# Kernel tuning notes

Measured on AMD Instinct MI355X. Metric: run time of the kernel, lower is better.

Reference implementation:

```python
import jax, jax.numpy as jnp
import numpy as np

BN_EPS = 1e-5

def conv1x1(x_bcn, w, b):
    # x: [B,C,N], w: [O,C], b: [O] -> [B,O,N]
    return jnp.einsum('oc,bcn->bon', w, x_bcn) + b[None, :, None]

def bn_eval(x, g, b):
    # inference BN with running_mean=0, running_var=1
    return x / jnp.sqrt(1.0 + BN_EPS) * g + b

def setup_inputs() -> dict:
    key = jax.random.key(0)
    ks = jax.random.split(key, 24)
    B, C, H, W = 2, 256, 64, 64
    Cq = C // 4
    s = lambda k, sh, fan: jax.random.normal(k, sh, jnp.float32) * (1.0 / np.sqrt(fan))
    inp = {
        'input1': jax.random.normal(ks[0], (B, C, H, W), jnp.float32),
        'input2': jax.random.normal(ks[1], (B, C, H, W), jnp.float32),
        'q1_w': s(ks[2], (Cq, C), C), 'q1_b': jnp.zeros((Cq,), jnp.float32),
        'k1_w': s(ks[3], (Cq, C), C), 'k1_b': jnp.zeros((Cq,), jnp.float32),
        'v1_w': s(ks[4], (C, C), C),  'v1_b': jnp.zeros((C,), jnp.float32),
        'q2_w': s(ks[5], (Cq, C), C), 'q2_b': jnp.zeros((Cq,), jnp.float32),
        'k2_w': s(ks[6], (Cq, C), C), 'k2_b': jnp.zeros((Cq,), jnp.float32),
        'v2_w': s(ks[7], (C, C), C),  'v2_b': jnp.zeros((C,), jnp.float32),
        'g1_w': s(ks[8], (C, 2 * C), 2 * C), 'g1_b': jnp.zeros((C,), jnp.float32),
        'bn1_g': jnp.ones((C,), jnp.float32), 'bn1_b': jnp.zeros((C,), jnp.float32),
        'g2_w': s(ks[9], (Cq, C), C), 'g2_b': jnp.zeros((Cq,), jnp.float32),
        'bn2_g': jnp.ones((Cq,), jnp.float32), 'bn2_b': jnp.zeros((Cq,), jnp.float32),
        'gamma': jnp.zeros((1,), jnp.float32) + 0.5,  # nonzero so attention branch matters
    }
    return inp

def _attshare(input1, input2, q1_w, q1_b, k1_w, k1_b, v1_w, v1_b,
              q2_w, q2_b, k2_w, k2_b, v2_w, v2_b,
              g1_w, g1_b, bn1_g, bn1_b, g2_w, g2_b, bn2_g, bn2_b, gamma):
    B, C, H, W = input1.shape
    N = H * W
    x1 = input1.reshape(B, C, N)
    x2 = input2.reshape(B, C, N)
    # global attention branch: adaptive avg pool -> conv -> BN -> relu -> conv -> BN -> sigmoid
    pooled = jnp.concatenate([x1, x2], axis=1).mean(axis=2)          # [B, 2C]
    y = jnp.einsum('oc,bc->bo', g1_w, pooled) + g1_b
    y = jax.nn.relu(bn_eval(y, bn1_g, bn1_b))
    y = jnp.einsum('oc,bc->bo', g2_w, y) + g2_b
    g = jax.nn.sigmoid(bn_eval(y, bn2_g, bn2_b))                      # [B, C/4]

    def stream(x, inp4d, qw, qb, kw, kb, vw, vb):
        q = conv1x1(x, qw, qb).transpose(0, 2, 1)   # [B, N, C/4]
        k = conv1x1(x, kw, kb)                       # [B, C/4, N]
        v = conv1x1(x, vw, vb)                       # [B, C, N]
        # bmm(q, g.repeat(N)) has identical columns -> per-row bias
        bias = jnp.einsum('bnc,bc->bn', q, g)        # [B, N]
        attn = jnp.einsum('bnc,bcm->bnm', q, k) + bias[:, :, None]
        attn = jax.nn.softmax(attn, axis=-1)         # [B, N, N]
        out = jnp.einsum('bcj,bij->bci', v, attn)    # [B, C, N]
        return gamma * out.reshape(inp4d.shape) + inp4d

    out1 = stream(x1, input1, q1_w, q1_b, k1_w, k1_b, v1_w, v1_b)
    out2 = stream(x2, input2, q2_w, q2_b, k2_w, k2_b, v2_w, v2_b)
    return out1, out2

def reference(input1, input2, q1_w, q1_b, k1_w, k1_b, v1_w, v1_b,
              q2_w, q2_b, k2_w, k2_b, v2_w, v2_b,
              g1_w, g1_b, bn1_g, bn1_b, g2_w, g2_b, bn2_g, bn2_b, gamma):
    return _attshare(input1, input2, q1_w, q1_b, k1_w, k1_b, v1_w, v1_b,
                     q2_w, q2_b, k2_w, k2_b, v2_w, v2_b,
                     g1_w, g1_b, bn1_g, bn1_b, g2_w, g2_b, bn2_g, bn2_b, gamma)
```

## Files before the change

### kernel.cpp

```cpp
#include <hip/hip_runtime.h>
#include <math.h>

constexpr int B_  = 2;
constexpr int C_  = 256;
constexpr int CQ_ = 64;
constexpr int N_  = 4096;

typedef __attribute__((ext_vector_type(8))) short     short8;
typedef __attribute__((ext_vector_type(8))) _Float16  half8;
typedef __attribute__((ext_vector_type(4))) float     f32x4;

constexpr float SHIFT = 24.0f;

static __device__ __forceinline__ unsigned short f2bf(float x) {
    union { float f; unsigned u; } v; v.f = x;
    unsigned r = (v.u + 0x7FFFu + ((v.u >> 16) & 1u)) >> 16;
    return (unsigned short)r;
}

__global__ __launch_bounds__(256)
void wconv_kernel(const float* __restrict__ q1w, const float* __restrict__ k1w,
                  const float* __restrict__ v1w, const float* __restrict__ q2w,
                  const float* __restrict__ k2w, const float* __restrict__ v2w,
                  _Float16* __restrict__ wb)
{
    int i = (blockIdx.x * 256 + threadIdx.x) * 4;
    const float* src;
    int off;
    if      (i < 16384)  { src = q1w; off = 0; }
    else if (i < 32768)  { src = k1w; off = 16384; }
    else if (i < 98304)  { src = v1w; off = 32768; }
    else if (i < 114688) { src = q2w; off = 98304; }
    else if (i < 131072) { src = k2w; off = 114688; }
    else                 { src = v2w; off = 131072; }
    float4 f = *(const float4*)(src + (i - off));
    _Float16 h0 = (_Float16)f.x, h1 = (_Float16)f.y;
    _Float16 h2 = (_Float16)f.z, h3 = (_Float16)f.w;
    ushort4 u;
    u.x = *(unsigned short*)&h0; u.y = *(unsigned short*)&h1;
    u.z = *(unsigned short*)&h2; u.w = *(unsigned short*)&h3;
    *(ushort4*)((unsigned short*)wb + i) = u;
}

__global__ __launch_bounds__(512)
void proj_kernel(const float* __restrict__ in1, const float* __restrict__ in2,
                 const _Float16* __restrict__ wb,
                 const float* __restrict__ q1b, const float* __restrict__ k1b,
                 const float* __restrict__ v1b, const float* __restrict__ q2b,
                 const float* __restrict__ k2b, const float* __restrict__ v2b,
                 _Float16* __restrict__ q_ws, _Float16* __restrict__ kf_ws,
                 unsigned short* __restrict__ vf_ws)
{
    __shared__ _Float16 Xs[64 * 264];
    const int bs = blockIdx.y, s = bs >> 1, bb = bs & 1;
    const int n0 = blockIdx.x * 64;
    const float* x = (s ? in2 : in1) + (size_t)bb * C_ * N_;
    const int tid = threadIdx.x;
    const int lane = tid & 63, wave = tid >> 6, quad = lane >> 4, l15 = lane & 15;

    #pragma unroll
    for (int rep = 0; rep < 8; ++rep) {
        int idx = rep * 512 + tid;
        int c = idx >> 4, ng = idx & 15;
        float4 f = *(const float4*)(x + (size_t)c * N_ + n0 + ng * 4);
        Xs[(ng * 4 + 0) * 264 + c] = (_Float16)f.x;
        Xs[(ng * 4 + 1) * 264 + c] = (_Float16)f.y;
        Xs[(ng * 4 + 2) * 264 + c] = (_Float16)f.z;
        Xs[(ng * 4 + 3) * 264 + c] = (_Float16)f.w;
    }
    __syncthreads();

    const _Float16* wqs = wb + (size_t)s * 98304;
    const _Float16* wks = wqs + 16384;
    const _Float16* wvs = wks + 16384;

    {
        const int m = wave >> 2, nb = wave & 3;
        const _Float16* W = m ? wks : wqs;
        const float* bias = m ? (s ? k2b : k1b) : (s ? q2b : q1b);
        half8 af[8];
        #pragma unroll
        for (int kh = 0; kh < 8; ++kh)
            af[kh] = *(const half8*)(&Xs[(16 * nb + l15) * 264 + quad * 8 + kh * 32]);
        f32x4 a4[4];
        #pragma unroll
        for (int o = 0; o < 4; ++o) a4[o] = (f32x4){0.f, 0.f, 0.f, 0.f};
        #pragma unroll
        for (int kh = 0; kh < 8; ++kh)
            #pragma unroll
            for (int o = 0; o < 4; ++o) {
                half8 bf = *(const half8*)(W + (size_t)(16 * o + l15) * C_ + quad * 8 + kh * 32);
                a4[o] = __builtin_amdgcn_mfma_f32_16x16x32_f16(af[kh], bf, a4[o], 0, 0, 0);
            }
        if (m == 0) {
            _Float16* outp = q_ws + (size_t)bs * N_ * CQ_;
            #pragma unroll
            for (int o = 0; o < 4; ++o) {
                float bv = bias[16 * o + l15];
                #pragma unroll
                for (int r = 0; r < 4; ++r) {
                    int n = n0 + 16 * nb + quad * 4 + r;
                    outp[(size_t)n * CQ_ + 16 * o + l15] = (_Float16)(a4[o][r] + bv);
                }
            }
        } else {
            unsigned short* kd = (unsigned short*)(kf_ws) + (size_t)bs * 262144;
            const int jt = (n0 >> 4) + nb;
            const int e = l15 & 7;
            #pragma unroll
            for (int o = 0; o < 4; ++o) {
                float bv = bias[16 * o + l15];
                const int kh = o >> 1;
                const int lhi = ((o & 1) * 2 + (l15 >> 3)) * 16;
                #pragma unroll
                for (int r = 0; r < 4; ++r) {
                    _Float16 hv = (_Float16)(a4[o][r] + bv);
                    int lane_f = lhi + quad * 4 + r;
                    kd[(size_t)(jt * 2 + kh) * 512 + lane_f * 8 + e] = *(unsigned short*)&hv;
                }
            }
        }
    }

    {
        const float* vb = s ? v2b : v1b;
        unsigned short* vd = vf_ws + (size_t)bs * 1048576;
        f32x4 v4[2][4];
        #pragma unroll
        for (int o = 0; o < 2; ++o)
            #pragma unroll
            for (int nt = 0; nt < 4; ++nt) v4[o][nt] = (f32x4){0.f, 0.f, 0.f, 0.f};
        #pragma unroll
        for (int kh = 0; kh < 8; ++kh) {
            half8 bf[4], af[2];
            #pragma unroll
            for (int nt = 0; nt < 4; ++nt)
                bf[nt] = *(const half8*)(&Xs[(16 * nt + l15) * 264 + quad * 8 + kh * 32]);
            #pragma unroll
            for (int o = 0; o < 2; ++o)
                af[o] = *(const half8*)(wvs + (size_t)(32 * wave + 16 * o + l15) * C_ + quad * 8 + kh * 32);
            #pragma unroll
            for (int o = 0; o < 2; ++o)
                #pragma unroll
                for (int nt = 0; nt < 4; ++nt)
                    v4[o][nt] = __builtin_amdgcn_mfma_f32_16x16x32_f16(af[o], bf[nt], v4[o][nt], 0, 0, 0);
        }
        const int e = l15 & 7;
        #pragma unroll
        for (int o = 0; o < 2; ++o) {
            const int ct = 2 * wave + o;
            #pragma unroll
            for (int r = 0; r < 4; ++r) {
                int c = 32 * wave + 16 * o + quad * 4 + r;
                float bv = vb[c];
                #pragma unroll
                for (int nt = 0; nt < 4; ++nt) {
                    const int j32 = (n0 >> 5) + (nt >> 1);
                    const int lane_f = ((nt & 1) * 2 + (l15 >> 3)) * 16 + quad * 4 + r;
                    vd[(size_t)(j32 * 16 + ct) * 512 + lane_f * 8 + e] =
                        f2bf(v4[o][nt][r] + bv);
                }
            }
        }
    }
}

__global__ __launch_bounds__(1024)
void flash_kernel(const _Float16* __restrict__ qg,
                  const _Float16* __restrict__ kfg,
                  const unsigned short* __restrict__ vfg,
                  const float* __restrict__ in1, const float* __restrict__ in2,
                  const float* __restrict__ gamma_p, float* __restrict__ out)
{
    __shared__ unsigned short Pt[2][64 * 64];
    __shared__ float lsum[64 * 4];

    const int tid  = threadIdx.x;
    const int lane = tid & 63;
    const int wave = tid >> 6;
    const int quad = lane >> 4;
    const int l15  = lane & 15;
    const int bs   = blockIdx.x & 3;
    const int q0   = (blockIdx.x >> 2) * 64;
    const int s = bs >> 1, bb = bs & 1;
    const int jsub  = wave & 3;
    const int ihalf = (wave >> 2) & 1;
    const int wc = wave & 7;
    const int jh = wave >> 3;

    const _Float16* qp = qg + (size_t)bs * N_ * CQ_;
    const _Float16* kB = kfg + (size_t)bs * 262144 + lane * 8;
    const unsigned short* vB = vfg + (size_t)bs * 1048576 + (size_t)lane * 8;

    unsigned char* ptb0 = (unsigned char*)&Pt[0][0];
    unsigned char* ptb1 = (unsigned char*)&Pt[1][0];

    half8 qf[2][2];
    float lacc[2] = {0.f, 0.f};
    half8 kf[2];
    short8 vf[2];
    f32x4 acc[4][2];
    #pragma unroll
    for (int a = 0; a < 4; ++a)
        #pragma unroll
        for (int bq = 0; bq < 2; ++bq) acc[a][bq] = (f32x4){0.f, 0.f, 0.f, 0.f};

    if (wave < 8) {
        #pragma unroll
        for (int isub = 0; isub < 2; ++isub)
            #pragma unroll
            for (int kh = 0; kh < 2; ++kh)
                qf[isub][kh] = *(const half8*)(
                    qp + (size_t)(q0 + 32 * ihalf + 16 * isub + l15) * CQ_ + quad * 8 + kh * 32);
        kf[0] = *(const half8*)(kB + (size_t)(jsub * 2 + 0) * 512);
        kf[1] = *(const half8*)(kB + (size_t)(jsub * 2 + 1) * 512);
        f32x4 sacc[2];
        sacc[0] = (f32x4){0.f, 0.f, 0.f, 0.f};
        sacc[1] = (f32x4){0.f, 0.f, 0.f, 0.f};
        #pragma unroll
        for (int kh = 0; kh < 2; ++kh)
            #pragma unroll
            for (int isub = 0; isub < 2; ++isub)
                sacc[isub] = __builtin_amdgcn_mfma_f32_16x16x32_f16(
                    kf[kh], qf[isub][kh], sacc[isub], 0, 0, 0);
        #pragma unroll
        for (int isub = 0; isub < 2; ++isub) {
            f32x4 p;
            p.x = __expf(sacc[isub].x - SHIFT);
            p.y = __expf(sacc[isub].y - SHIFT);
            p.z = __expf(sacc[isub].z - SHIFT);
            p.w = __expf(sacc[isub].w - SHIFT);
            lacc[isub] += p.x + p.y + p.z + p.w;
            unsigned pk0, pk1;
            asm("v_cvt_pk_bf16_f32 %0, %1, %2" : "=v"(pk0) : "v"(p.x), "v"(p.y));
            asm("v_cvt_pk_bf16_f32 %0, %1, %2" : "=v"(pk1) : "v"(p.z), "v"(p.w));
            int row = 32 * ihalf + 16 * isub + l15;
            int cb  = (32 * jsub + 8 * quad) ^ ((row & 7) << 4);
            uint2 pbv; pbv.x = pk0; pbv.y = pk1;
            *(uint2*)(ptb0 + row * 128 + cb) = pbv;
        }
        kf[0] = *(const half8*)(kB + (size_t)((4 + jsub) * 2 + 0) * 512);
        kf[1] = *(const half8*)(kB + (size_t)((4 + jsub) * 2 + 1) * 512);
    }
    vf[0] = *(const short8*)(vB + (size_t)(jh * 16 + 2 * wc + 0) * 512);
    vf[1] = *(const short8*)(vB + (size_t)(jh * 16 + 2 * wc + 1) * 512);

    for (int t = 0; t < 64; ++t) {
        unsigned char* ptr = (t & 1) ? ptb1 : ptb0;
        unsigned char* ptw = (t & 1) ? ptb0 : ptb1;

        asm volatile("s_waitcnt lgkmcnt(0)" ::: "memory");
        __builtin_amdgcn_sched_barrier(0);
        __builtin_amdgcn_s_barrier();
        __builtin_amdgcn_sched_barrier(0);

        short8 ap[4];
        #pragma unroll
        for (int is2 = 0; is2 < 4; ++is2) {
            int row = 16 * is2 + l15;
            int cb  = (jh * 64 + quad * 16) ^ ((row & 7) << 4);
            ap[is2] = *(const short8*)(ptr + row * 128 + cb);
        }
        __builtin_amdgcn_s_setprio(1);
        #pragma unroll
        for (int is2 = 0; is2 < 4; ++is2)
            #pragma unroll
            for (int csub = 0; csub < 2; ++csub)
                acc[is2][csub] = __builtin_amdgcn_mfma_f32_16x16x32_bf16(
                    ap[is2], vf[csub], acc[is2][csub], 0, 0, 0);
        __builtin_amdgcn_s_setprio(0);

        if (t < 63) {
            if (wave < 8) {
                f32x4 sacc[2];
                sacc[0] = (f32x4){0.f, 0.f, 0.f, 0.f};
                sacc[1] = (f32x4){0.f, 0.f, 0.f, 0.f};
                #pragma unroll
                for (int kh = 0; kh < 2; ++kh)
                    #pragma unroll
                    for (int isub = 0; isub < 2; ++isub)
                        sacc[isub] = __builtin_amdgcn_mfma_f32_16x16x32_f16(
                            kf[kh], qf[isub][kh], sacc[isub], 0, 0, 0);
                #pragma unroll
                for (int isub = 0; isub < 2; ++isub) {
                    f32x4 p;
                    p.x = __expf(sacc[isub].x - SHIFT);
                    p.y = __expf(sacc[isub].y - SHIFT);
                    p.z = __expf(sacc[isub].z - SHIFT);
                    p.w = __expf(sacc[isub].w - SHIFT);
                    lacc[isub] += p.x + p.y + p.z + p.w;
                    unsigned pk0, pk1;
                    asm("v_cvt_pk_bf16_f32 %0, %1, %2" : "=v"(pk0) : "v"(p.x), "v"(p.y));
                    asm("v_cvt_pk_bf16_f32 %0, %1, %2" : "=v"(pk1) : "v"(p.z), "v"(p.w));
                    int row = 32 * ihalf + 16 * isub + l15;
                    int cb  = (32 * jsub + 8 * quad) ^ ((row & 7) << 4);
                    uint2 pbv; pbv.x = pk0; pbv.y = pk1;
                    *(uint2*)(ptw + row * 128 + cb) = pbv;
                }
                int tk = (t + 2) & 63;
                kf[0] = *(const half8*)(kB + (size_t)((tk * 4 + jsub) * 2 + 0) * 512);
                kf[1] = *(const half8*)(kB + (size_t)((tk * 4 + jsub) * 2 + 1) * 512);
            }
            vf[0] = *(const short8*)(vB + (size_t)((2 * (t + 1) + jh) * 16 + 2 * wc + 0) * 512);
            vf[1] = *(const short8*)(vB + (size_t)((2 * (t + 1) + jh) * 16 + 2 * wc + 1) * 512);
        }
    }

    if (wave < 8) {
        #pragma unroll
        for (int isub = 0; isub < 2; ++isub) {
            float t = lacc[isub];
            t += __shfl_xor(t, 16);
            t += __shfl_xor(t, 32);
            if (quad == 0)
                lsum[(32 * ihalf + 16 * isub + l15) * 4 + jsub] = t;
        }
    }
    __syncthreads();

    float* red = (float*)&Pt[0][0];
    #pragma unroll
    for (int r = 0; r < 4; ++r) {
        if (wave >= 8) {
            *(f32x4*)(red + (size_t)(wave - 8) * 512 + lane * 8 + 0) = acc[r][0];
            *(f32x4*)(red + (size_t)(wave - 8) * 512 + lane * 8 + 4) = acc[r][1];
        }
        __syncthreads();
        if (wave < 8) {
            f32x4 a0 = *(const f32x4*)(red + (size_t)wave * 512 + lane * 8 + 0);
            f32x4 a1 = *(const f32x4*)(red + (size_t)wave * 512 + lane * 8 + 4);
            acc[r][0] += a0;
            acc[r][1] += a1;
        }
        __syncthreads();
    }

    if (wave < 8) {
        const float gamma = gamma_p[0];
        const float* inp = (s ? in2 : in1) + (size_t)bb * C_ * N_;
        float* op = out + (size_t)bs * C_ * N_;
        #pragma unroll
        for (int is2 = 0; is2 < 4; ++is2) {
            float inv[4];
            #pragma unroll
            for (int r = 0; r < 4; ++r) {
                f32x4 t = *(const f32x4*)(&lsum[(16 * is2 + quad * 4 + r) * 4]);
                inv[r] = 1.0f / (t.x + t.y + t.z + t.w);
            }
            const int i0 = q0 + 16 * is2 + 4 * quad;
            #pragma unroll
            for (int csub = 0; csub < 2; ++csub) {
                const int c = 32 * wc + 16 * csub + l15;
                const size_t idx = (size_t)c * N_ + i0;
                float4 r4 = *(const float4*)(inp + idx);
                float4 o4;
                o4.x = gamma * acc[is2][csub][0] * inv[0] + r4.x;
                o4.y = gamma * acc[is2][csub][1] * inv[1] + r4.y;
                o4.z = gamma * acc[is2][csub][2] * inv[2] + r4.z;
                o4.w = gamma * acc[is2][csub][3] * inv[3] + r4.w;
                *(float4*)(op + idx) = o4;
            }
        }
    }
}

extern "C" void kernel_launch(void* const* d_in, const int* in_sizes, int n_in,
                              void* d_out, int out_size, void* d_ws, size_t ws_size,
                              hipStream_t stream)
{
    const float* in1 = (const float*)d_in[0];
    const float* in2 = (const float*)d_in[1];
    const float* q1w = (const float*)d_in[2];
    const float* q1b = (const float*)d_in[3];
    const float* k1w = (const float*)d_in[4];
    const float* k1b = (const float*)d_in[5];
    const float* v1w = (const float*)d_in[6];
    const float* v1b = (const float*)d_in[7];
    const float* q2w = (const float*)d_in[8];
    const float* q2b = (const float*)d_in[9];
    const float* k2w = (const float*)d_in[10];
    const float* k2b = (const float*)d_in[11];
    const float* v2w = (const float*)d_in[12];
    const float* v2b = (const float*)d_in[13];
    const float* gamma = (const float*)d_in[22];
    float* out = (float*)d_out;

    _Float16* wb   = (_Float16*)d_ws;
    _Float16* q_ws = wb + 196608;
    _Float16* kf_ws = q_ws + (size_t)4 * N_ * CQ_;
    unsigned short* vf_ws = (unsigned short*)(kf_ws + (size_t)4 * 262144);

    wconv_kernel<<<dim3(192), 256, 0, stream>>>(q1w, k1w, v1w, q2w, k2w, v2w, wb);
    proj_kernel<<<dim3(64, 4), 512, 0, stream>>>(
        in1, in2, wb, q1b, k1b, v1b, q2b, k2b, v2b, q_ws, kf_ws, vf_ws);
    flash_kernel<<<dim3(256), 1024, 0, stream>>>(
        q_ws, kf_ws, vf_ws, in1, in2, gamma, out);
}
```

Baseline: 178.2 us.

## Specialize waves into score producers and PV consumers in flash kernel

Splits the 16 waves into roles. Waves 0-7 only compute QK scores, exp and write P tiles to shared memory. Waves 8-15 only do the P·V MFMAs, each now covering 64 channels (4 csub) instead of 32, so all 16 waves no longer share the PV work. The final reduction pairs consumer waves by jh instead of folding into the producer waves. The K prefetch also moves earlier, ahead of the exp. This is meant to overlap softmax and PV work across waves, but it doubles the accumulator registers per consumer wave and halves the number of waves doing PV MFMAs.

```diff
diff --git a/kernel.cpp b/kernel.cpp
--- a/kernel.cpp
+++ b/kernel.cpp
@@ -183,10 +183,6 @@
     const int bs   = blockIdx.x & 3;
     const int q0   = (blockIdx.x >> 2) * 64;
     const int s = bs >> 1, bb = bs & 1;
-    const int jsub  = wave & 3;
-    const int ihalf = (wave >> 2) & 1;
-    const int wc = wave & 7;
-    const int jh = wave >> 3;
 
     const _Float16* qp = qg + (size_t)bs * N_ * CQ_;
     const _Float16* kB = kfg + (size_t)bs * 262144 + lane * 8;
@@ -195,17 +191,18 @@
     unsigned char* ptb0 = (unsigned char*)&Pt[0][0];
     unsigned char* ptb1 = (unsigned char*)&Pt[1][0];
 
-    half8 qf[2][2];
-    float lacc[2] = {0.f, 0.f};
-    half8 kf[2];
-    short8 vf[2];
-    f32x4 acc[4][2];
-    #pragma unroll
-    for (int a = 0; a < 4; ++a)
-        #pragma unroll
-        for (int bq = 0; bq < 2; ++bq) acc[a][bq] = (f32x4){0.f, 0.f, 0.f, 0.f};
+    f32x4 acc[4][4];
+    const int pw  = wave - 8;
+    const int jh  = pw & 1;
+    const int wc4 = pw >> 1;
 
     if (wave < 8) {
+        const int jsub  = wave & 3;
+        const int ihalf = (wave >> 2) & 1;
+        half8 qf[2][2];
+        half8 kf[2];
+        float lacc[2] = {0.f, 0.f};
+
         #pragma unroll
         for (int isub = 0; isub < 2; ++isub)
             #pragma unroll
@@ -214,64 +211,43 @@
                     qp + (size_t)(q0 + 32 * ihalf + 16 * isub + l15) * CQ_ + quad * 8 + kh * 32);
         kf[0] = *(const half8*)(kB + (size_t)(jsub * 2 + 0) * 512);
         kf[1] = *(const half8*)(kB + (size_t)(jsub * 2 + 1) * 512);
-        f32x4 sacc[2];
-        sacc[0] = (f32x4){0.f, 0.f, 0.f, 0.f};
-        sacc[1] = (f32x4){0.f, 0.f, 0.f, 0.f};
-        #pragma unroll
-        for (int kh = 0; kh < 2; ++kh)
-            #pragma unroll
-            for (int isub = 0; isub < 2; ++isub)
-                sacc[isub] = __builtin_amdgcn_mfma_f32_16x16x32_f16(
-                    kf[kh], qf[isub][kh], sacc[isub], 0, 0, 0);
-        #pragma unroll
-        for (int isub = 0; isub < 2; ++isub) {
-            f32x4 p;
-            p.x = __expf(sacc[isub].x - SHIFT);
-            p.y = __expf(sacc[isub].y - SHIFT);
-            p.z = __expf(sacc[isub].z - SHIFT);
-            p.w = __expf(sacc[isub].w - SHIFT);
-            lacc[isub] += p.x + p.y + p.z + p.w;
-            unsigned pk0, pk1;
-            asm("v_cvt_pk_bf16_f32 %0, %1, %2" : "=v"(pk0) : "v"(p.x), "v"(p.y));
-            asm("v_cvt_pk_bf16_f32 %0, %1, %2" : "=v"(pk1) : "v"(p.z), "v"(p.w));
-            int row = 32 * ihalf + 16 * isub + l15;
-            int cb  = (32 * jsub + 8 * quad) ^ ((row & 7) << 4);
-            uint2 pbv; pbv.x = pk0; pbv.y = pk1;
-            *(uint2*)(ptb0 + row * 128 + cb) = pbv;
+        {
+            f32x4 sacc[2];
+            sacc[0] = (f32x4){0.f, 0.f, 0.f, 0.f};
+            sacc[1] = (f32x4){0.f, 0.f, 0.f, 0.f};
+            #pragma unroll
+            for (int kh = 0; kh < 2; ++kh)
+                #pragma unroll
+                for (int isub = 0; isub < 2; ++isub)
+                    sacc[isub] = __builtin_amdgcn_mfma_f32_16x16x32_f16(
+                        kf[kh], qf[isub][kh], sacc[isub], 0, 0, 0);
+            #pragma unroll
+            for (int isub = 0; isub < 2; ++isub) {
+                f32x4 p;
+                p.x = __expf(sacc[isub].x - SHIFT);
+                p.y = __expf(sacc[isub].y - SHIFT);
+                p.z = __expf(sacc[isub].z - SHIFT);
+                p.w = __expf(sacc[isub].w - SHIFT);
+                lacc[isub] += p.x + p.y + p.z + p.w;
+                unsigned pk0, pk1;
+                asm("v_cvt_pk_bf16_f32 %0, %1, %2" : "=v"(pk0) : "v"(p.x), "v"(p.y));
+                asm("v_cvt_pk_bf16_f32 %0, %1, %2" : "=v"(pk1) : "v"(p.z), "v"(p.w));
+                int row = 32 * ihalf + 16 * isub + l15;
+                int cb  = (32 * jsub + 8 * quad) ^ ((row & 7) << 4);
+                uint2 pbv; pbv.x = pk0; pbv.y = pk1;
+                *(uint2*)(ptb0 + row * 128 + cb) = pbv;
+            }
         }
         kf[0] = *(const half8*)(kB + (size_t)((4 + jsub) * 2 + 0) * 512);
         kf[1] = *(const half8*)(kB + (size_t)((4 + jsub) * 2 + 1) * 512);
-    }
-    vf[0] = *(const short8*)(vB + (size_t)(jh * 16 + 2 * wc + 0) * 512);
-    vf[1] = *(const short8*)(vB + (size_t)(jh * 16 + 2 * wc + 1) * 512);
-
-    for (int t = 0; t < 64; ++t) {
-        unsigned char* ptr = (t & 1) ? ptb1 : ptb0;
-        unsigned char* ptw = (t & 1) ? ptb0 : ptb1;
-
-        asm volatile("s_waitcnt lgkmcnt(0)" ::: "memory");
-        __builtin_amdgcn_sched_barrier(0);
-        __builtin_amdgcn_s_barrier();
-        __builtin_amdgcn_sched_barrier(0);
-
-        short8 ap[4];
-        #pragma unroll
-        for (int is2 = 0; is2 < 4; ++is2) {
-            int row = 16 * is2 + l15;
-            int cb  = (jh * 64 + quad * 16) ^ ((row & 7) << 4);
-            ap[is2] = *(const short8*)(ptr + row * 128 + cb);
-        }
-        __builtin_amdgcn_s_setprio(1);
-        #pragma unroll
-        for (int is2 = 0; is2 < 4; ++is2)
-            #pragma unroll
-            for (int csub = 0; csub < 2; ++csub)
-                acc[is2][csub] = __builtin_amdgcn_mfma_f32_16x16x32_bf16(
-                    ap[is2], vf[csub], acc[is2][csub], 0, 0, 0);
-        __builtin_amdgcn_s_setprio(0);
-
-        if (t < 63) {
-            if (wave < 8) {
+
+        for (int t = 0; t < 64; ++t) {
+            asm volatile("s_waitcnt lgkmcnt(0)" ::: "memory");
+            __builtin_amdgcn_sched_barrier(0);
+            __builtin_amdgcn_s_barrier();
+            __builtin_amdgcn_sched_barrier(0);
+            if (t < 63) {
+                unsigned char* ptw = (t & 1) ? ptb0 : ptb1;
                 f32x4 sacc[2];
                 sacc[0] = (f32x4){0.f, 0.f, 0.f, 0.f};
                 sacc[1] = (f32x4){0.f, 0.f, 0.f, 0.f};
@@ -281,6 +257,9 @@
                     for (int isub = 0; isub < 2; ++isub)
                         sacc[isub] = __builtin_amdgcn_mfma_f32_16x16x32_f16(
                             kf[kh], qf[isub][kh], sacc[isub], 0, 0, 0);
+                int tk = (t + 2) & 63;
+                half8 kn0 = *(const half8*)(kB + (size_t)((tk * 4 + jsub) * 2 + 0) * 512);
+                half8 kn1 = *(const half8*)(kB + (size_t)((tk * 4 + jsub) * 2 + 1) * 512);
                 #pragma unroll
                 for (int isub = 0; isub < 2; ++isub) {
                     f32x4 p;
@@ -297,16 +276,10 @@
                     uint2 pbv; pbv.x = pk0; pbv.y = pk1;
                     *(uint2*)(ptw + row * 128 + cb) = pbv;
                 }
-                int tk = (t + 2) & 63;
-                kf[0] = *(const half8*)(kB + (size_t)((tk * 4 + jsub) * 2 + 0) * 512);
-                kf[1] = *(const half8*)(kB + (size_t)((tk * 4 + jsub) * 2 + 1) * 512);
-            }
-            vf[0] = *(const short8*)(vB + (size_t)((2 * (t + 1) + jh) * 16 + 2 * wc + 0) * 512);
-            vf[1] = *(const short8*)(vB + (size_t)((2 * (t + 1) + jh) * 16 + 2 * wc + 1) * 512);
-        }
-    }
-
-    if (wave < 8) {
+                kf[0] = kn0; kf[1] = kn1;
+            }
+        }
+
         #pragma unroll
         for (int isub = 0; isub < 2; ++isub) {
             float t = lacc[isub];
@@ -315,27 +288,69 @@
             if (quad == 0)
                 lsum[(32 * ihalf + 16 * isub + l15) * 4 + jsub] = t;
         }
+    } else {
+        #pragma unroll
+        for (int a = 0; a < 4; ++a)
+            #pragma unroll
+            for (int bq = 0; bq < 4; ++bq) acc[a][bq] = (f32x4){0.f, 0.f, 0.f, 0.f};
+        short8 vf[4];
+        #pragma unroll
+        for (int csub = 0; csub < 4; ++csub)
+            vf[csub] = *(const short8*)(vB + (size_t)(jh * 16 + 4 * wc4 + csub) * 512);
+
+        for (int t = 0; t < 64; ++t) {
+            unsigned char* ptr = (t & 1) ? ptb1 : ptb0;
+            asm volatile("s_waitcnt lgkmcnt(0)" ::: "memory");
+            __builtin_amdgcn_sched_barrier(0);
+            __builtin_amdgcn_s_barrier();
+            __builtin_amdgcn_sched_barrier(0);
+
+            short8 ap[4];
+            #pragma unroll
+            for (int is2 = 0; is2 < 4; ++is2) {
+                int row = 16 * is2 + l15;
+                int cb  = (jh * 64 + quad * 16) ^ ((row & 7) << 4);
+                ap[is2] = *(const short8*)(ptr + row * 128 + cb);
+            }
+            __builtin_amdgcn_s_setprio(1);
+            #pragma unroll
+            for (int is2 = 0; is2 < 4; ++is2)
+                #pragma unroll
+                for (int csub = 0; csub < 4; ++csub)
+                    acc[is2][csub] = __builtin_amdgcn_mfma_f32_16x16x32_bf16(
+                        ap[is2], vf[csub], acc[is2][csub], 0, 0, 0);
+            __builtin_amdgcn_s_setprio(0);
+
+            if (t < 63) {
+                #pragma unroll
+                for (int csub = 0; csub < 4; ++csub)
+                    vf[csub] = *(const short8*)(
+                        vB + (size_t)((2 * (t + 1) + jh) * 16 + 4 * wc4 + csub) * 512);
+            }
+        }
     }
     __syncthreads();
 
     float* red = (float*)&Pt[0][0];
     #pragma unroll
-    for (int r = 0; r < 4; ++r) {
-        if (wave >= 8) {
-            *(f32x4*)(red + (size_t)(wave - 8) * 512 + lane * 8 + 0) = acc[r][0];
-            *(f32x4*)(red + (size_t)(wave - 8) * 512 + lane * 8 + 4) = acc[r][1];
+    for (int rr = 0; rr < 4; ++rr) {
+        if (wave >= 8 && (wave & 1)) {
+            const int slot = (wave - 9) >> 1;
+            #pragma unroll
+            for (int q = 0; q < 4; ++q)
+                *(f32x4*)(red + (size_t)slot * 1024 + lane * 16 + q * 4) = acc[rr][q];
         }
         __syncthreads();
-        if (wave < 8) {
-            f32x4 a0 = *(const f32x4*)(red + (size_t)wave * 512 + lane * 8 + 0);
-            f32x4 a1 = *(const f32x4*)(red + (size_t)wave * 512 + lane * 8 + 4);
-            acc[r][0] += a0;
-            acc[r][1] += a1;
+        if (wave >= 8 && !(wave & 1)) {
+            const int slot = (wave - 8) >> 1;
+            #pragma unroll
+            for (int q = 0; q < 4; ++q)
+                acc[rr][q] += *(const f32x4*)(red + (size_t)slot * 1024 + lane * 16 + q * 4);
         }
         __syncthreads();
     }
 
-    if (wave < 8) {
+    if (wave >= 8 && !(wave & 1)) {
         const float gamma = gamma_p[0];
         const float* inp = (s ? in2 : in1) + (size_t)bb * C_ * N_;
         float* op = out + (size_t)bs * C_ * N_;
@@ -349,8 +364,8 @@
             }
             const int i0 = q0 + 16 * is2 + 4 * quad;
             #pragma unroll
-            for (int csub = 0; csub < 2; ++csub) {
-                const int c = 32 * wc + 16 * csub + l15;
+            for (int csub = 0; csub < 4; ++csub) {
+                const int c = 64 * wc4 + 16 * csub + l15;
                 const size_t idx = (size_t)c * N_ + i0;
                 float4 r4 = *(const float4*)(inp + idx);
                 float4 o4;
```

New measurement: 175.7 us. About the same (-1.4%).
